# Kernel tuning notes

Measured on AMD Instinct MI355X. Metric: run time of the kernel, lower is better.

Reference implementation:

```python
import jax, jax.numpy as jnp
import numpy as np

G, N, E = 16, 512, 2048        # graphs, nodes/graph, edges/graph
CN, CE = 64, 64                # node / edge feature channels
K = 3                          # Laguerre polynomial order
RATIO = 0.5
KEEP = int(np.ceil(RATIO * N)) # 256 kept nodes per graph (static)
POWER_ITERS = 64               # power iteration approximating eigsh(k=1,'LM')


def setup_inputs() -> dict:
    key = jax.random.key(0)
    ks = jax.random.split(key, 10)
    x_n = jax.random.normal(ks[0], (G * N, CN), jnp.float32)
    x_e = jax.random.normal(ks[1], (G * E, CE), jnp.float32)
    # incidence endpoints per edge, local node ids, no self loops
    u = jax.random.randint(ks[2], (G, E), 0, N)
    v = (u + 1 + jax.random.randint(ks[3], (G, E), 0, N - 1)) % N
    # node-level conv graph (global ids within per-graph blocks): both directions
    offs = (jnp.arange(G) * N)[:, None]
    src_n = jnp.concatenate([(u + offs).reshape(-1), (v + offs).reshape(-1)])
    dst_n = jnp.concatenate([(v + offs).reshape(-1), (u + offs).reshape(-1)])
    edge_weight_n = jax.random.uniform(ks[4], (src_n.shape[0],), jnp.float32)
    # edge-level conv graph (global ids within per-graph edge blocks)
    ME = 4 * E
    offs_e = (jnp.arange(G) * E)[:, None]
    src_e = (jax.random.randint(ks[5], (G, ME), 0, E) + offs_e).reshape(-1)
    dst_e = (jax.random.randint(ks[6], (G, ME), 0, E) + offs_e).reshape(-1)
    edge_weight_e = jax.random.uniform(ks[7], (src_e.shape[0],), jnp.float32)
    # HodgeLaguerreConv(C -> 1, K) weights (glorot-ish) + bias (zeros init)
    W_n = jax.random.normal(ks[8], (K, CN), jnp.float32) / np.sqrt(CN)
    b_n = jnp.zeros((1,), jnp.float32)
    W_e = jax.random.normal(ks[9], (K, CE), jnp.float32) / np.sqrt(CE)
    b_e = jnp.zeros((1,), jnp.float32)
    return dict(x_n=x_n, x_e=x_e, edge_u=u, edge_v=v,
                src_n=src_n, dst_n=dst_n, edge_weight_n=edge_weight_n,
                src_e=src_e, dst_e=dst_e, edge_weight_e=edge_weight_e,
                W_n=W_n, b_n=b_n, W_e=W_e, b_e=b_e)


def hodge_laguerre(x, src, dst, w, Wk, b):
    """HodgeLaguerreConv with out_channels=1: out = sum_k T_k(L) x @ Wk[k] + b.
    T_0 = x; T_1 = x - Lx; T_{k+1} = (-L T_k + (2k+1) T_k - k T_{k-1})/(k+1)."""
    num = x.shape[0]
    def L(z):  # scatter-add message passing: out[i] = sum_{j->i} norm * z[j]
        return jax.ops.segment_sum(w[:, None] * z[src], dst, num_segments=num)
    Tx0 = x
    out = Tx0 @ Wk[0]
    Tx1 = x - L(x)
    out = out + Tx1 @ Wk[1]
    k = 1
    for i in range(2, Wk.shape[0]):
        Tx2 = (-L(Tx1) + (2 * k + 1) * Tx1 - k * Tx0) / (k + 1)
        out = out + Tx2 @ Wk[i]
        Tx0, Tx1 = Tx1, Tx2
        k += 1
    return out + b[0]


def pool_graph(sn, se, xn, xe, u, v):
    # node score augmented by |B1| @ edge_score (abs incidence gathers both endpoints)
    aug = sn.at[u].add(se).at[v].add(se)
    perm = jnp.argsort(-aug)                    # descending sort, take top KEEP
    mask_n = jnp.zeros((N,), xn.dtype).at[perm[:KEEP]].set(1.0)
    # mask_e = |B1|^T (1 - mask_n); keep edge iff both endpoints kept (== 0)
    bad = (1.0 - mask_n[u]) + (1.0 - mask_n[v])
    keep_e = (bad == 0.0).astype(xn.dtype)
    # dense incidence B1 [N, E]: -1 at source row, +1 at target row
    cols = jnp.arange(E)
    B = jnp.zeros((N, E), xn.dtype).at[u, cols].add(-1.0).at[v, cols].add(1.0)
    Bm = B * mask_n[:, None] * keep_e[None, :]  # row/col masking (zero-padded)
    L0 = Bm @ Bm.T                              # [N, N] node Laplacian
    L1 = Bm.T @ Bm                              # [E, E] edge Laplacian
    # power iteration for lambda_max(L0) (== eigsh k=1 'LM'; zero rows keep spectrum)
    w = jnp.ones((N,), xn.dtype) / np.sqrt(N)
    for _ in range(POWER_ITERS):
        w = L0 @ w
        w = w / (jnp.linalg.norm(w) + 1e-12)
    lam = w @ (L0 @ w)
    scale = 2.0 / (lam + 1e-12)
    return xn * mask_n[:, None], L0 * scale, xe * keep_e[:, None], L1 * scale


def reference(x_n, x_e, edge_u, edge_v, src_n, dst_n, edge_weight_n,
              src_e, dst_e, edge_weight_e, W_n, b_n, W_e, b_e):
    score_n = jax.nn.sigmoid(hodge_laguerre(x_n, src_n, dst_n, edge_weight_n, W_n, b_n).reshape(-1))
    score_e = jax.nn.sigmoid(hodge_laguerre(x_e, src_e, dst_e, edge_weight_e, W_e, b_e).reshape(-1))
    xn_g = (x_n * score_n[:, None]).reshape(G, N, CN)
    xe_g = (x_e * score_e[:, None]).reshape(G, E, CE)
    sn = score_n.reshape(G, N)
    se = score_e.reshape(G, E)
    return jax.vmap(pool_graph)(sn, se, xn_g, xe_g, edge_u, edge_v)
```

## Files before the change

### kernel.cpp

```cpp
#include <hip/hip_runtime.h>
#include <math.h>

#define GG 16
#define NNODE 512
#define EEDGE 2048
#define KEEPN 256
#define PITERS 64

#define NNT (GG*NNODE)
#define NET (GG*EEDGE)
#define MN (2*GG*EEDGE)
#define ME (4*GG*EEDGE)

#define WS_C1N 0
#define WS_C2N 8192
#define WS_BN  16384
#define WS_D1N 24576
#define WS_D2N 32768
#define WS_E2N 40960
#define WS_SN  49152
#define WS_C1E 57344
#define WS_C2E 90112
#define WS_BE  122880
#define WS_D1E 155648
#define WS_D2E 188416
#define WS_E2E 221184
#define WS_SE  253952
#define WS_MASK 286720
#define WS_KEEP 294912
#define WS_KLIST 327680
#define WS_KCNT 360448
#define WS_SCALE 360464
#define WS_TOTAL 360480

#define O_XN 0
#define O_L0 524288
#define O_XE 4718592
#define O_L1 6815744

__global__ __launch_bounds__(256) void k_dots(const float* __restrict__ xn,
    const float* __restrict__ xe, const float* __restrict__ Wn,
    const float* __restrict__ We, float* __restrict__ ws) {
  int gw = (blockIdx.x * 256 + threadIdx.x) >> 6;
  int lane = threadIdx.x & 63;
  const float* x; const float* W; int row; float *c1, *c2, *bs;
  if (gw < NNT) {
    row = gw; x = xn + (size_t)row * 64; W = Wn;
    c1 = ws + WS_C1N; c2 = ws + WS_C2N; bs = ws + WS_BN;
  } else {
    row = gw - NNT; if (row >= NET) return;
    x = xe + (size_t)row * 64; W = We;
    c1 = ws + WS_C1E; c2 = ws + WS_C2E; bs = ws + WS_BE;
  }
  float v = x[lane];
  float r0 = v * W[lane];
  float r1 = v * W[64 + lane];
  float r2 = v * W[128 + lane];
  for (int o = 32; o; o >>= 1) {
    r0 += __shfl_xor(r0, o, 64);
    r1 += __shfl_xor(r1, o, 64);
    r2 += __shfl_xor(r2, o, 64);
  }
  if (lane == 0) { c1[row] = r1; c2[row] = r2; bs[row] = r0 + r1 + r2; }
}

__global__ __launch_bounds__(256) void k_scat1(
    const int* __restrict__ sn, const int* __restrict__ dn, const float* __restrict__ wn,
    const int* __restrict__ se, const int* __restrict__ de, const float* __restrict__ we,
    float* __restrict__ ws) {
  int t = blockIdx.x * 256 + threadIdx.x;
  if (t < MN) {
    int s = sn[t], d = dn[t]; float w = wn[t];
    atomicAdd(ws + WS_D1N + d, w * ws[WS_C1N + s]);
    atomicAdd(ws + WS_D2N + d, w * ws[WS_C2N + s]);
  } else {
    int t2 = t - MN; if (t2 >= ME) return;
    int s = se[t2], d = de[t2]; float w = we[t2];
    atomicAdd(ws + WS_D1E + d, w * ws[WS_C1E + s]);
    atomicAdd(ws + WS_D2E + d, w * ws[WS_C2E + s]);
  }
}

__global__ __launch_bounds__(256) void k_scat2(
    const int* __restrict__ sn, const int* __restrict__ dn, const float* __restrict__ wn,
    const int* __restrict__ se, const int* __restrict__ de, const float* __restrict__ we,
    float* __restrict__ ws) {
  int t = blockIdx.x * 256 + threadIdx.x;
  if (t < MN) {
    int s = sn[t], d = dn[t]; float w = wn[t];
    atomicAdd(ws + WS_E2N + d, w * ws[WS_D2N + s]);
  } else {
    int t2 = t - MN; if (t2 >= ME) return;
    int s = se[t2], d = de[t2]; float w = we[t2];
    atomicAdd(ws + WS_E2E + d, w * ws[WS_D2E + s]);
  }
}

__global__ __launch_bounds__(512) void k_fat(
    const int* __restrict__ edge_u, const int* __restrict__ edge_v,
    const float* __restrict__ bn, const float* __restrict__ be,
    float* __restrict__ ws, float* __restrict__ out, int nzb) {
  const int tid = threadIdx.x;
  if (blockIdx.x >= 16) {
    const long long L04 = 4194304 / 4;
    const long long TOT4 = (4194304LL + 67108864LL) / 4;
    float4 z4 = make_float4(0.f, 0.f, 0.f, 0.f);
    float4* o4 = (float4*)out;
    long long start = (long long)(blockIdx.x - 16) * 512 + tid;
    long long stride = (long long)nzb * 512;
    for (long long i = start; i < TOT4; i += stride) {
      long long f = (i < L04) ? (O_L0 / 4 + i) : (O_L1 / 4 + (i - L04));
      o4[f] = z4;
    }
    return;
  }
  const int g = blockIdx.x;
  __shared__ float aug[NNODE];
  __shared__ float key[NNODE];
  __shared__ int kidx[NNODE];
  __shared__ int su[EEDGE];
  __shared__ int sv[EEDGE];
  __shared__ int maskS[NNODE];
  __shared__ int degS[NNODE];
  __shared__ int offS[NNODE];
  __shared__ int adj[2 * EEDGE];
  __shared__ float wv[NNODE];
  __shared__ float red[8];
  __shared__ int kcnt;
  int* wsi = (int*)ws;

  float bn0 = bn[0], be0 = be[0];
  int nidx = g * NNODE + tid;
  {
    float t = ws[WS_BN + nidx] - ws[WS_D1N + nidx] - 2.0f * ws[WS_D2N + nidx]
            + 0.5f * ws[WS_E2N + nidx] + bn0;
    float s = 1.0f / (1.0f + expf(-t));
    ws[WS_SN + nidx] = s;
    aug[tid] = s;
  }
  for (int e = tid; e < EEDGE; e += 512) {
    su[e] = edge_u[g * EEDGE + e];
    sv[e] = edge_v[g * EEDGE + e];
  }
  if (tid == 0) kcnt = 0;
  maskS[tid] = 0;
  __syncthreads();
  for (int e = tid; e < EEDGE; e += 512) {
    int eidx = g * EEDGE + e;
    float t = ws[WS_BE + eidx] - ws[WS_D1E + eidx] - 2.0f * ws[WS_D2E + eidx]
            + 0.5f * ws[WS_E2E + eidx] + be0;
    float s = 1.0f / (1.0f + expf(-t));
    ws[WS_SE + eidx] = s;
    atomicAdd(&aug[su[e]], s);
    atomicAdd(&aug[sv[e]], s);
  }
  __syncthreads();
  key[tid] = aug[tid]; kidx[tid] = tid;
  __syncthreads();
  for (int k = 2; k <= NNODE; k <<= 1) {
    for (int j = k >> 1; j > 0; j >>= 1) {
      int i = tid, ixj = i ^ j;
      if (ixj > i) {
        float ka = key[i], kb = key[ixj];
        int ia = kidx[i], ib = kidx[ixj];
        bool aAfter = (ka < kb) || (ka == kb && ia > ib);
        bool doswap = ((i & k) == 0) ? aAfter : !aAfter;
        if (doswap) { key[i] = kb; key[ixj] = ka; kidx[i] = ib; kidx[ixj] = ia; }
      }
      __syncthreads();
    }
  }
  if (tid < KEEPN) maskS[kidx[tid]] = 1;
  degS[tid] = 0;
  __syncthreads();
  wsi[WS_MASK + nidx] = maskS[tid];
  for (int e = tid; e < EEDGE; e += 512) {
    int k = maskS[su[e]] & maskS[sv[e]];
    wsi[WS_KEEP + g * EEDGE + e] = k;
    if (k) {
      int p = atomicAdd(&kcnt, 1);
      wsi[WS_KLIST + g * EEDGE + p] = e;
      atomicAdd(&degS[su[e]], 1);
      atomicAdd(&degS[sv[e]], 1);
    }
  }
  __syncthreads();
  if (tid == 0) wsi[WS_KCNT + g] = kcnt;
  int* t0 = (int*)key;
  t0[tid] = degS[tid];
  __syncthreads();
  for (int s = 1; s < NNODE; s <<= 1) {
    int v = t0[tid] + ((tid >= s) ? t0[tid - s] : 0);
    __syncthreads();
    t0[tid] = v;
    __syncthreads();
  }
  offS[tid] = t0[tid] - degS[tid];
  __syncthreads();
  for (int e = tid; e < EEDGE; e += 512) {
    if (maskS[su[e]] & maskS[sv[e]]) {
      int pu = atomicAdd(&offS[su[e]], 1); adj[pu] = sv[e];
      int pv = atomicAdd(&offS[sv[e]], 1); adj[pv] = su[e];
    }
  }
  __syncthreads();
  int myDeg = degS[tid];
  int myEnd = offS[tid];
  int myStart = myEnd - myDeg;
  const int lane = tid & 63;
  const int wvid = tid >> 6;
  wv[tid] = 0.04419417382415922f;
  __syncthreads();
  for (int it = 0; it < PITERS; ++it) {
    float acc = (float)myDeg * wv[tid];
    for (int p = myStart; p < myEnd; ++p) acc -= wv[adj[p]];
    float sq = acc * acc;
    for (int o = 32; o; o >>= 1) sq += __shfl_xor(sq, o, 64);
    if (lane == 0) red[wvid] = sq;
    __syncthreads();
    float tot = red[0] + red[1] + red[2] + red[3] + red[4] + red[5] + red[6] + red[7];
    float rn = 1.0f / (sqrtf(tot) + 1e-12f);
    wv[tid] = acc * rn;
    __syncthreads();
  }
  {
    float acc = (float)myDeg * wv[tid];
    for (int p = myStart; p < myEnd; ++p) acc -= wv[adj[p]];
    float pr = wv[tid] * acc;
    for (int o = 32; o; o >>= 1) pr += __shfl_xor(pr, o, 64);
    if (lane == 0) red[wvid] = pr;
    __syncthreads();
    if (tid == 0) {
      float lam = red[0] + red[1] + red[2] + red[3] + red[4] + red[5] + red[6] + red[7];
      ws[WS_SCALE + g] = 2.0f / (lam + 1e-12f);
    }
  }
}

__global__ __launch_bounds__(256) void k_out(
    const float* __restrict__ xn, const float* __restrict__ xe,
    const int* __restrict__ edge_u, const int* __restrict__ edge_v,
    const float* __restrict__ ws, float* __restrict__ out) {
  int b = blockIdx.x, tid = threadIdx.x;
  const int* wsi = (const int*)ws;
  if (b < 512) {
    int idx = b * 256 + tid;
    int row = idx >> 4;
    float s = ws[WS_SN + row] * (float)wsi[WS_MASK + row];
    float4 x4 = ((const float4*)xn)[idx];
    float4 r = make_float4(x4.x * s, x4.y * s, x4.z * s, x4.w * s);
    ((float4*)(out + O_XN))[idx] = r;
  } else if (b < 2560) {
    int idx = (b - 512) * 256 + tid;
    int row = idx >> 4;
    float s = ws[WS_SE + row] * (float)wsi[WS_KEEP + row];
    float4 x4 = ((const float4*)xe)[idx];
    float4 r = make_float4(x4.x * s, x4.y * s, x4.z * s, x4.w * s);
    ((float4*)(out + O_XE))[idx] = r;
  } else if (b < 2576) {
    int g = b - 2560;
    int cnt = wsi[WS_KCNT + g];
    float s = ws[WS_SCALE + g];
    float* L0 = out + O_L0 + (long long)g * (NNODE * NNODE);
    const int* kl = wsi + WS_KLIST + g * EEDGE;
    const int* eu = edge_u + g * EEDGE;
    const int* ev = edge_v + g * EEDGE;
    for (int t = tid; t < cnt; t += 256) {
      int e = kl[t];
      int u = eu[e], v = ev[e];
      atomicAdd(&L0[u * NNODE + u], s);
      atomicAdd(&L0[v * NNODE + v], s);
      atomicAdd(&L0[u * NNODE + v], -s);
      atomicAdd(&L0[v * NNODE + u], -s);
    }
  } else {
    int q = b - 2576;
    int g = q >> 8, sb = q & 255;
    int cnt = wsi[WS_KCNT + g];
    float s = ws[WS_SCALE + g];
    float* L1 = out + O_L1 + (long long)g * (EEDGE * EEDGE);
    const int* kl = wsi + WS_KLIST + g * EEDGE;
    const int* eu = edge_u + g * EEDGE;
    const int* ev = edge_v + g * EEDGE;
    for (int a = sb; a < cnt; a += 256) {
      int e1 = kl[a];
      int u1 = eu[e1], v1 = ev[e1];
      long long rowoff = (long long)e1 * EEDGE;
      for (int b2 = tid; b2 < cnt; b2 += 256) {
        int e2 = kl[b2];
        int u2 = eu[e2], v2 = ev[e2];
        int val = (u1 == u2) + (v1 == v2) - (v1 == u2) - (u1 == v2);
        if (val) L1[rowoff + e2] = s * (float)val;
      }
    }
  }
}

extern "C" void kernel_launch(void* const* d_in, const int* in_sizes, int n_in,
                              void* d_out, int out_size, void* d_ws, size_t ws_size,
                              hipStream_t stream) {
  const float* x_n = (const float*)d_in[0];
  const float* x_e = (const float*)d_in[1];
  const int* edge_u = (const int*)d_in[2];
  const int* edge_v = (const int*)d_in[3];
  const int* src_n = (const int*)d_in[4];
  const int* dst_n = (const int*)d_in[5];
  const float* ew_n = (const float*)d_in[6];
  const int* src_e = (const int*)d_in[7];
  const int* dst_e = (const int*)d_in[8];
  const float* ew_e = (const float*)d_in[9];
  const float* W_n = (const float*)d_in[10];
  const float* b_n = (const float*)d_in[11];
  const float* W_e = (const float*)d_in[12];
  const float* b_e = (const float*)d_in[13];
  float* ws = (float*)d_ws;
  float* out = (float*)d_out;

  hipMemsetAsync(d_ws, 0, (size_t)WS_TOTAL * sizeof(float), stream);
  k_dots<<<(NNT + NET) / 4, 256, 0, stream>>>(x_n, x_e, W_n, W_e, ws);
  k_scat1<<<(MN + ME) / 256, 256, 0, stream>>>(src_n, dst_n, ew_n, src_e, dst_e, ew_e, ws);
  k_scat2<<<(MN + ME) / 256, 256, 0, stream>>>(src_n, dst_n, ew_n, src_e, dst_e, ew_e, ws);
  const int nzb = 2048;
  k_fat<<<16 + nzb, 512, 0, stream>>>(edge_u, edge_v, b_n, b_e, ws, out, nzb);
  k_out<<<6672, 256, 0, stream>>>(x_n, x_e, edge_u, edge_v, ws, out);
}
```

Before: 470.7 us.

## Per-graph shared-memory message passing and spread Laplacian zeroing across kernels

Replaces the two global-atomic scatter kernels with one per-graph kernel. It keeps the C1/C2 coefficients and the D1/D2/E2 accumulators in LDS, computes the sigmoid scores there, and removes the workspace memset. The large zero-fill of the L0/L1 output is split into three ranges and placed in extra blocks of k_dots, k_msg and k_pool, so it overlaps with the dependent small stages. The trade-off is that only 32 blocks do the message passing, one per graph per level, each walking up to 8192 edges, which limits parallelism for that phase.

New measurement: 513.2 us. 1.09x slower.

```diff
diff --git a/kernel.cpp b/kernel.cpp
--- a/kernel.cpp
+++ b/kernel.cpp
@@ -6,41 +6,50 @@
 #define EEDGE 2048
 #define KEEPN 256
 #define PITERS 64
-
-#define NNT (GG*NNODE)
-#define NET (GG*EEDGE)
-#define MN (2*GG*EEDGE)
-#define ME (4*GG*EEDGE)
+#define NNT 8192
+#define NET 32768
 
 #define WS_C1N 0
 #define WS_C2N 8192
 #define WS_BN  16384
-#define WS_D1N 24576
-#define WS_D2N 32768
-#define WS_E2N 40960
-#define WS_SN  49152
-#define WS_C1E 57344
-#define WS_C2E 90112
-#define WS_BE  122880
-#define WS_D1E 155648
-#define WS_D2E 188416
-#define WS_E2E 221184
-#define WS_SE  253952
-#define WS_MASK 286720
-#define WS_KEEP 294912
-#define WS_KLIST 327680
-#define WS_KCNT 360448
-#define WS_SCALE 360464
-#define WS_TOTAL 360480
+#define WS_SN  24576
+#define WS_C1E 32768
+#define WS_C2E 65536
+#define WS_BE  98304
+#define WS_SE  131072
+#define WS_MASK 163840
+#define WS_KEEP 172032
+#define WS_KLIST 204800
+#define WS_KCNT 237568
+#define WS_SCALE 237584
 
 #define O_XN 0
 #define O_L0 524288
 #define O_XE 4718592
 #define O_L1 6815744
 
+#define L04 1048576
+#define ZTOT4 17825792
+#define ZB1 7340032
+#define ZB2 14680064
+
+__device__ __forceinline__ void zero_range(float* __restrict__ out, int lo, int hi,
+                                           int start, int stride) {
+  float4 z = make_float4(0.f, 0.f, 0.f, 0.f);
+  float4* o4 = (float4*)out;
+  for (int i = lo + start; i < hi; i += stride) {
+    int f = (i < L04) ? (O_L0 / 4 + i) : (O_L1 / 4 + (i - L04));
+    o4[f] = z;
+  }
+}
+
 __global__ __launch_bounds__(256) void k_dots(const float* __restrict__ xn,
     const float* __restrict__ xe, const float* __restrict__ Wn,
-    const float* __restrict__ We, float* __restrict__ ws) {
+    const float* __restrict__ We, float* __restrict__ ws, float* __restrict__ out) {
+  if (blockIdx.x >= 10240) {
+    zero_range(out, 0, ZB1, (blockIdx.x - 10240) * 256 + threadIdx.x, 262144);
+    return;
+  }
   int gw = (blockIdx.x * 256 + threadIdx.x) >> 6;
   int lane = threadIdx.x & 63;
   const float* x; const float* W; int row; float *c1, *c2, *bs;
@@ -48,7 +57,7 @@
     row = gw; x = xn + (size_t)row * 64; W = Wn;
     c1 = ws + WS_C1N; c2 = ws + WS_C2N; bs = ws + WS_BN;
   } else {
-    row = gw - NNT; if (row >= NET) return;
+    row = gw - NNT;
     x = xe + (size_t)row * 64; W = We;
     c1 = ws + WS_C1E; c2 = ws + WS_C2E; bs = ws + WS_BE;
   }
@@ -64,54 +73,69 @@
   if (lane == 0) { c1[row] = r1; c2[row] = r2; bs[row] = r0 + r1 + r2; }
 }
 
-__global__ __launch_bounds__(256) void k_scat1(
-    const int* __restrict__ sn, const int* __restrict__ dn, const float* __restrict__ wn,
-    const int* __restrict__ se, const int* __restrict__ de, const float* __restrict__ we,
-    float* __restrict__ ws) {
-  int t = blockIdx.x * 256 + threadIdx.x;
-  if (t < MN) {
-    int s = sn[t], d = dn[t]; float w = wn[t];
-    atomicAdd(ws + WS_D1N + d, w * ws[WS_C1N + s]);
-    atomicAdd(ws + WS_D2N + d, w * ws[WS_C2N + s]);
-  } else {
-    int t2 = t - MN; if (t2 >= ME) return;
-    int s = se[t2], d = de[t2]; float w = we[t2];
-    atomicAdd(ws + WS_D1E + d, w * ws[WS_C1E + s]);
-    atomicAdd(ws + WS_D2E + d, w * ws[WS_C2E + s]);
-  }
-}
-
-__global__ __launch_bounds__(256) void k_scat2(
-    const int* __restrict__ sn, const int* __restrict__ dn, const float* __restrict__ wn,
-    const int* __restrict__ se, const int* __restrict__ de, const float* __restrict__ we,
-    float* __restrict__ ws) {
-  int t = blockIdx.x * 256 + threadIdx.x;
-  if (t < MN) {
-    int s = sn[t], d = dn[t]; float w = wn[t];
-    atomicAdd(ws + WS_E2N + d, w * ws[WS_D2N + s]);
-  } else {
-    int t2 = t - MN; if (t2 >= ME) return;
-    int s = se[t2], d = de[t2]; float w = we[t2];
-    atomicAdd(ws + WS_E2E + d, w * ws[WS_D2E + s]);
-  }
-}
-
-__global__ __launch_bounds__(512) void k_fat(
+__global__ __launch_bounds__(256) void k_msg(
+    const int* __restrict__ src_n, const int* __restrict__ dst_n, const float* __restrict__ wn,
+    const int* __restrict__ src_e, const int* __restrict__ dst_e, const float* __restrict__ we,
+    const float* __restrict__ bnp, const float* __restrict__ bep,
+    float* __restrict__ ws, float* __restrict__ out) {
+  if (blockIdx.x >= 32) {
+    zero_range(out, ZB1, ZB2, (blockIdx.x - 32) * 256 + threadIdx.x, 262144);
+    return;
+  }
+  __shared__ float sm[5 * 2048];
+  float* c1 = sm;
+  float* c2 = sm + 2048;
+  float* d1 = sm + 4096;
+  float* d2 = sm + 6144;
+  float* e2 = sm + 8192;
+  const int tid = threadIdx.x;
+  const bool isNode = blockIdx.x < 16;
+  const int g = isNode ? blockIdx.x : blockIdx.x - 16;
+  const int n = isNode ? NNODE : EEDGE;
+  const int roff = g * n;
+  const float* C1 = ws + (isNode ? WS_C1N : WS_C1E) + roff;
+  const float* C2 = ws + (isNode ? WS_C2N : WS_C2E) + roff;
+  const float* BB = ws + (isNode ? WS_BN : WS_BE) + roff;
+  float* S = ws + (isNode ? WS_SN : WS_SE) + roff;
+  const float bias = isNode ? bnp[0] : bep[0];
+  const int ecnt = isNode ? 4096 : 8192;
+  const int* SA = isNode ? src_n : src_e;
+  const int* DA = isNode ? dst_n : dst_e;
+  const float* WA = isNode ? wn : we;
+
+  for (int i = tid; i < n; i += 256) {
+    c1[i] = C1[i]; c2[i] = C2[i]; d1[i] = 0.f; d2[i] = 0.f; e2[i] = 0.f;
+  }
+  __syncthreads();
+  for (int t = tid; t < ecnt; t += 256) {
+    int idx = isNode ? ((t < 2048) ? g * 2048 + t : 32768 + g * 2048 + (t - 2048))
+                     : g * 8192 + t;
+    int s = SA[idx] - roff, d = DA[idx] - roff;
+    float w = WA[idx];
+    atomicAdd(&d1[d], w * c1[s]);
+    atomicAdd(&d2[d], w * c2[s]);
+  }
+  __syncthreads();
+  for (int t = tid; t < ecnt; t += 256) {
+    int idx = isNode ? ((t < 2048) ? g * 2048 + t : 32768 + g * 2048 + (t - 2048))
+                     : g * 8192 + t;
+    int s = SA[idx] - roff, d = DA[idx] - roff;
+    float w = WA[idx];
+    atomicAdd(&e2[d], w * d2[s]);
+  }
+  __syncthreads();
+  for (int i = tid; i < n; i += 256) {
+    float t = BB[i] - d1[i] - 2.0f * d2[i] + 0.5f * e2[i] + bias;
+    S[i] = 1.0f / (1.0f + expf(-t));
+  }
+}
+
+__global__ __launch_bounds__(512) void k_pool(
     const int* __restrict__ edge_u, const int* __restrict__ edge_v,
-    const float* __restrict__ bn, const float* __restrict__ be,
-    float* __restrict__ ws, float* __restrict__ out, int nzb) {
+    float* __restrict__ ws, float* __restrict__ out) {
   const int tid = threadIdx.x;
   if (blockIdx.x >= 16) {
-    const long long L04 = 4194304 / 4;
-    const long long TOT4 = (4194304LL + 67108864LL) / 4;
-    float4 z4 = make_float4(0.f, 0.f, 0.f, 0.f);
-    float4* o4 = (float4*)out;
-    long long start = (long long)(blockIdx.x - 16) * 512 + tid;
-    long long stride = (long long)nzb * 512;
-    for (long long i = start; i < TOT4; i += stride) {
-      long long f = (i < L04) ? (O_L0 / 4 + i) : (O_L1 / 4 + (i - L04));
-      o4[f] = z4;
-    }
+    zero_range(out, ZB2, ZTOT4, (blockIdx.x - 16) * 512 + tid, 262144);
     return;
   }
   const int g = blockIdx.x;
@@ -129,15 +153,8 @@
   __shared__ int kcnt;
   int* wsi = (int*)ws;
 
-  float bn0 = bn[0], be0 = be[0];
   int nidx = g * NNODE + tid;
-  {
-    float t = ws[WS_BN + nidx] - ws[WS_D1N + nidx] - 2.0f * ws[WS_D2N + nidx]
-            + 0.5f * ws[WS_E2N + nidx] + bn0;
-    float s = 1.0f / (1.0f + expf(-t));
-    ws[WS_SN + nidx] = s;
-    aug[tid] = s;
-  }
+  aug[tid] = ws[WS_SN + nidx];
   for (int e = tid; e < EEDGE; e += 512) {
     su[e] = edge_u[g * EEDGE + e];
     sv[e] = edge_v[g * EEDGE + e];
@@ -146,11 +163,7 @@
   maskS[tid] = 0;
   __syncthreads();
   for (int e = tid; e < EEDGE; e += 512) {
-    int eidx = g * EEDGE + e;
-    float t = ws[WS_BE + eidx] - ws[WS_D1E + eidx] - 2.0f * ws[WS_D2E + eidx]
-            + 0.5f * ws[WS_E2E + eidx] + be0;
-    float s = 1.0f / (1.0f + expf(-t));
-    ws[WS_SE + eidx] = s;
+    float s = ws[WS_SE + g * EEDGE + e];
     atomicAdd(&aug[su[e]], s);
     atomicAdd(&aug[sv[e]], s);
   }
@@ -248,15 +261,13 @@
     int row = idx >> 4;
     float s = ws[WS_SN + row] * (float)wsi[WS_MASK + row];
     float4 x4 = ((const float4*)xn)[idx];
-    float4 r = make_float4(x4.x * s, x4.y * s, x4.z * s, x4.w * s);
-    ((float4*)(out + O_XN))[idx] = r;
+    ((float4*)(out + O_XN))[idx] = make_float4(x4.x * s, x4.y * s, x4.z * s, x4.w * s);
   } else if (b < 2560) {
     int idx = (b - 512) * 256 + tid;
     int row = idx >> 4;
     float s = ws[WS_SE + row] * (float)wsi[WS_KEEP + row];
     float4 x4 = ((const float4*)xe)[idx];
-    float4 r = make_float4(x4.x * s, x4.y * s, x4.z * s, x4.w * s);
-    ((float4*)(out + O_XE))[idx] = r;
+    ((float4*)(out + O_XE))[idx] = make_float4(x4.x * s, x4.y * s, x4.z * s, x4.w * s);
   } else if (b < 2576) {
     int g = b - 2560;
     int cnt = wsi[WS_KCNT + g];
@@ -316,11 +327,9 @@
   float* ws = (float*)d_ws;
   float* out = (float*)d_out;
 
-  hipMemsetAsync(d_ws, 0, (size_t)WS_TOTAL * sizeof(float), stream);
-  k_dots<<<(NNT + NET) / 4, 256, 0, stream>>>(x_n, x_e, W_n, W_e, ws);
-  k_scat1<<<(MN + ME) / 256, 256, 0, stream>>>(src_n, dst_n, ew_n, src_e, dst_e, ew_e, ws);
-  k_scat2<<<(MN + ME) / 256, 256, 0, stream>>>(src_n, dst_n, ew_n, src_e, dst_e, ew_e, ws);
-  const int nzb = 2048;
-  k_fat<<<16 + nzb, 512, 0, stream>>>(edge_u, edge_v, b_n, b_e, ws, out, nzb);
+  k_dots<<<10240 + 1024, 256, 0, stream>>>(x_n, x_e, W_n, W_e, ws, out);
+  k_msg<<<32 + 1024, 256, 0, stream>>>(src_n, dst_n, ew_n, src_e, dst_e, ew_e,
+                                       b_n, b_e, ws, out);
+  k_pool<<<16 + 512, 512, 0, stream>>>(edge_u, edge_v, ws, out);
   k_out<<<6672, 256, 0, stream>>>(x_n, x_e, edge_u, edge_v, ws, out);
 }
```
